# Optimization experiments

Hardware: AMD Instinct MI355X
Metric: run time of the kernel (lower is better)

Reference implementation:

```python
import jax, jax.numpy as jnp
import numpy as np

B, N, M = 2, 2048, 2048
D = 1024          # query_dim == context_dim == inner_dim
H, DH = 16, 64    # heads, dim_head
SCALE = DH ** -0.5


def setup_inputs() -> dict:
    key = jax.random.key(0)
    ks = jax.random.split(key, 7)
    s = 0.02
    return {
        "x": jax.random.normal(ks[0], (B, N, D), jnp.float32),
        "context": jax.random.normal(ks[1], (B, M, D), jnp.float32),
        "Wq": jax.random.normal(ks[2], (D, H * DH), jnp.float32) * s,
        "Wk": jax.random.normal(ks[3], (D, H * DH), jnp.float32) * s,
        "Wv": jax.random.normal(ks[4], (D, H * DH), jnp.float32) * s,
        "Wo": jax.random.normal(ks[5], (H * DH, D), jnp.float32) * s,
        "bo": jax.random.normal(ks[6], (D,), jnp.float32) * s,
    }


def reference(x, context, Wq, Wk, Wv, Wo, bo):
    # Linear projections (bias-free, as in to_q/to_k/to_v)
    q = (x @ Wq).reshape(B, N, H, DH)        # [B,N,H,DH]
    k = (context @ Wk).reshape(B, M, H, DH)  # [B,M,H,DH]
    v = (context @ Wv).reshape(B, M, H, DH)
    # QK^T * scale, softmax over keys, then AV
    sim = jnp.einsum('bnhd,bmhd->bhnm', q, k) * SCALE  # [B,H,N,M]
    attn = jax.nn.softmax(sim, axis=-1)
    out = jnp.einsum('bhnm,bmhd->bnhd', attn, v)       # [B,N,H,DH]
    out = out.reshape(B, N, H * DH)
    return out @ Wo + bo  # to_out Linear; dropout=0 is identity
```

## Files before the change

### kernel.cpp

```cpp
#include <hip/hip_runtime.h>

#define B_  2
#define N_  2048
#define M_  2048
#define D_  1024
#define H_  16
#define DH_ 64

typedef __bf16 bf16x8 __attribute__((ext_vector_type(8)));
typedef __bf16 bf16x4 __attribute__((ext_vector_type(4)));
typedef short  short4v __attribute__((ext_vector_type(4)));
typedef float  f32x4  __attribute__((ext_vector_type(4)));
typedef unsigned int u32x4v __attribute__((ext_vector_type(4)));

#define GAS(p) ((__attribute__((address_space(1))) void*)(p))
#define LAS(p) ((__attribute__((address_space(3))) void*)(p))

#define QPRESCALE 0.18033688011112042f

__device__ __forceinline__ unsigned short f2bf(float f) {
    unsigned int u = __builtin_bit_cast(unsigned int, f);
    u += 0x7fffu + ((u >> 16) & 1u);
    return (unsigned short)(u >> 16);
}

__device__ __forceinline__ unsigned cvtpkbf(float a, float b) {
    unsigned r;
    asm("v_cvt_pk_bf16_f32 %0, %1, %2" : "=v"(r) : "v"(a), "v"(b));
    return r;
}

__global__ __launch_bounds__(256) void prep(
    const float* __restrict__ x, const float* __restrict__ ctx,
    const float* __restrict__ Wq, const float* __restrict__ Wk,
    const float* __restrict__ Wv, const float* __restrict__ Wo,
    unsigned short* __restrict__ xb, unsigned short* __restrict__ cb,
    unsigned short* __restrict__ WTbase)
{
    if (blockIdx.z == 4) {
        int blk = blockIdx.y * 32 + blockIdx.x;
        int stride = 1024 * 256;
        for (int i = blk * 256 + threadIdx.x; i < 2097152; i += stride) {
            const float4* src; unsigned short* dst; int j;
            if (i < 1048576) { src = (const float4*)x;   dst = xb; j = i; }
            else             { src = (const float4*)ctx; dst = cb; j = i - 1048576; }
            float4 v = src[j];
            ushort4 o = make_ushort4(f2bf(v.x), f2bf(v.y), f2bf(v.z), f2bf(v.w));
            *(ushort4*)(dst + 4*j) = o;
        }
        return;
    }
    const float* W = (blockIdx.z == 0) ? Wq : (blockIdx.z == 1) ? Wk
                    : (blockIdx.z == 2) ? Wv : Wo;
    unsigned short* WT = WTbase + (size_t)blockIdx.z * 1048576;
    __shared__ unsigned short t[32][33];
    int tx = threadIdx.x & 31, ty8 = threadIdx.x >> 5;
    int c = blockIdx.x * 32 + tx;
#pragma unroll
    for (int i = 0; i < 4; ++i) {
        int r = blockIdx.y * 32 + i*8 + ty8;
        t[i*8 + ty8][tx] = f2bf(W[(size_t)r * 1024 + c]);
    }
    __syncthreads();
    int c2 = blockIdx.y * 32 + tx;
#pragma unroll
    for (int i = 0; i < 4; ++i) {
        int r2 = blockIdx.x * 32 + i*8 + ty8;
        WT[(size_t)r2 * 1024 + c2] = t[tx][i*8 + ty8];
    }
}

__global__ __launch_bounds__(256) void gemm128(
    const unsigned short* __restrict__ xb,
    const unsigned short* __restrict__ cb,
    const unsigned short* __restrict__ wT,
    const unsigned short* __restrict__ aoA,
    unsigned short* __restrict__ qkv_out,
    const float* __restrict__ bo,
    float* __restrict__ outF,
    int base_mode)
{
    __shared__ __align__(16) unsigned short As[128*32];
    __shared__ __align__(16) unsigned short Bs[128*32];

    const int mode = base_mode + blockIdx.z;
    const unsigned short* Amat;
    const unsigned short* Bt;
    if (mode == 0)      { Amat = wT;               Bt = xb; }
    else if (mode == 1) { Amat = wT + 1048576;     Bt = cb; }
    else if (mode == 2) { Amat = cb;               Bt = wT + 2*1048576; }
    else                { Amat = wT + 3*1048576;   Bt = aoA; }

    const int tid = threadIdx.x;
    const int w = tid >> 6, l = tid & 63;
    const int quad = l >> 4, l16 = l & 15;
    const int wm = w & 1, wn = w >> 1;
    int row0, col0;
    if (mode == 2) { row0 = blockIdx.x * 128; col0 = blockIdx.y * 128; }
    else           { row0 = blockIdx.y * 128; col0 = blockIdx.x * 128; }

    f32x4 acc[4][4];
#pragma unroll
    for (int i = 0; i < 4; ++i)
#pragma unroll
        for (int j = 0; j < 4; ++j) acc[i][j] = (f32x4){0.f, 0.f, 0.f, 0.f};

    for (int k0 = 0; k0 < 1024; k0 += 32) {
        __syncthreads();
#pragma unroll
        for (int i = 0; i < 2; ++i) {
            int s = i*256 + w*64 + l;
            int m = s >> 2, c = s & 3;
            int cs = c ^ ((m >> 1) & 3);
            __builtin_amdgcn_global_load_lds(
                GAS(Amat + (size_t)(row0 + m)*1024 + k0 + cs*8),
                LAS(As + (i*256 + w*64)*8), 16, 0, 0);
            __builtin_amdgcn_global_load_lds(
                GAS(Bt + (size_t)(col0 + m)*1024 + k0 + cs*8),
                LAS(Bs + (i*256 + w*64)*8), 16, 0, 0);
        }
        __syncthreads();

        bf16x8 af[4], bfr[4];
#pragma unroll
        for (int mt = 0; mt < 4; ++mt) {
            int m = wm*64 + mt*16 + l16;
            af[mt] = *reinterpret_cast<const bf16x8*>(As + m*32 + (quad ^ ((m >> 1) & 3))*8);
            int n = wn*64 + mt*16 + l16;
            bfr[mt] = *reinterpret_cast<const bf16x8*>(Bs + n*32 + (quad ^ ((n >> 1) & 3))*8);
        }
#pragma unroll
        for (int mt = 0; mt < 4; ++mt)
#pragma unroll
            for (int nt = 0; nt < 4; ++nt)
                acc[mt][nt] = __builtin_amdgcn_mfma_f32_16x16x32_bf16(
                    af[mt], bfr[nt], acc[mt][nt], 0, 0, 0);
    }

    if (mode == 3) {
#pragma unroll
        for (int mt = 0; mt < 4; ++mt) {
            int c = row0 + wm*64 + mt*16 + quad*4;
            float4 bv = *(const float4*)(bo + c);
#pragma unroll
            for (int nt = 0; nt < 4; ++nt) {
                int n = col0 + wn*64 + nt*16 + l16;
                float4 ov = make_float4(acc[mt][nt][0] + bv.x, acc[mt][nt][1] + bv.y,
                                        acc[mt][nt][2] + bv.z, acc[mt][nt][3] + bv.w);
                *(float4*)(outF + (size_t)n*1024 + c) = ov;
            }
        }
    } else if (mode == 2) {
#pragma unroll
        for (int mt = 0; mt < 4; ++mt) {
            int gr = row0 + wm*64 + mt*16 + quad*4;
            int b = gr >> 11, nidx = gr & 2047;
#pragma unroll
            for (int nt = 0; nt < 4; ++nt) {
                int col = col0 + wn*64 + nt*16 + l16;
                int h = col >> 6, d = col & 63;
                ushort4 pk = make_ushort4(f2bf(acc[mt][nt][0]), f2bf(acc[mt][nt][1]),
                                          f2bf(acc[mt][nt][2]), f2bf(acc[mt][nt][3]));
                *(ushort4*)(qkv_out + (size_t)2*4194304
                            + (size_t)((b*16 + h)*64 + d)*2048 + nidx) = pk;
            }
        }
    } else {
        const float qs = (mode == 0) ? QPRESCALE : 1.0f;
        unsigned short* obase = qkv_out + (size_t)mode*4194304;
#pragma unroll
        for (int nt = 0; nt < 4; ++nt) {
            int n = col0 + wn*64 + nt*16 + l16;
            int b = n >> 11, nidx = n & 2047;
#pragma unroll
            for (int mt = 0; mt < 4; ++mt) {
                int c = row0 + wm*64 + mt*16 + quad*4;
                int h = c >> 6, d = c & 63;
                ushort4 pkv = make_ushort4(
                    f2bf(acc[mt][nt][0] * qs), f2bf(acc[mt][nt][1] * qs),
                    f2bf(acc[mt][nt][2] * qs), f2bf(acc[mt][nt][3] * qs));
                *(ushort4*)(obase + (size_t)((b*16 + h)*2048 + nidx)*64 + d) = pkv;
            }
        }
    }
}

__global__ __launch_bounds__(256) void gemm_out(
    const unsigned short* __restrict__ woT,
    const unsigned short* __restrict__ aoA,
    const float* __restrict__ bo,
    float* __restrict__ outF)
{
    __shared__ __align__(16) unsigned short As[64*32];
    __shared__ __align__(16) unsigned short Bs[128*32];

    const int tid = threadIdx.x;
    const int w = tid >> 6, l = tid & 63;
    const int quad = l >> 4, l16 = l & 15;
    const int row0 = blockIdx.y * 64;
    const int col0 = blockIdx.x * 128;

    f32x4 acc[4][2];
#pragma unroll
    for (int i = 0; i < 4; ++i)
#pragma unroll
        for (int j = 0; j < 2; ++j) acc[i][j] = (f32x4){0.f, 0.f, 0.f, 0.f};

    for (int k0 = 0; k0 < 1024; k0 += 32) {
        __syncthreads();
        {
            int m = tid >> 2, c = tid & 3;
            int cs = c ^ ((m >> 1) & 3);
            __builtin_amdgcn_global_load_lds(
                GAS(woT + (size_t)(row0 + m)*1024 + k0 + cs*8),
                LAS(As + (w*64)*8), 16, 0, 0);
        }
#pragma unroll
        for (int i = 0; i < 2; ++i) {
            int s = i*256 + tid;
            int m = s >> 2, c = s & 3;
            int cs = c ^ ((m >> 1) & 3);
            __builtin_amdgcn_global_load_lds(
                GAS(aoA + (size_t)(col0 + m)*1024 + k0 + cs*8),
                LAS(Bs + (i*256 + w*64)*8), 16, 0, 0);
        }
        __syncthreads();

        bf16x8 af[4], bfr[2];
#pragma unroll
        for (int mt = 0; mt < 4; ++mt) {
            int m = mt*16 + l16;
            af[mt] = *reinterpret_cast<const bf16x8*>(As + m*32 + (quad ^ ((m >> 1) & 3))*8);
        }
#pragma unroll
        for (int nt = 0; nt < 2; ++nt) {
            int n = w*32 + nt*16 + l16;
            bfr[nt] = *reinterpret_cast<const bf16x8*>(Bs + n*32 + (quad ^ ((n >> 1) & 3))*8);
        }
#pragma unroll
        for (int mt = 0; mt < 4; ++mt)
#pragma unroll
            for (int nt = 0; nt < 2; ++nt)
                acc[mt][nt] = __builtin_amdgcn_mfma_f32_16x16x32_bf16(
                    af[mt], bfr[nt], acc[mt][nt], 0, 0, 0);
    }

#pragma unroll
    for (int mt = 0; mt < 4; ++mt) {
        int c = row0 + mt*16 + quad*4;
        float4 bv = *(const float4*)(bo + c);
#pragma unroll
        for (int nt = 0; nt < 2; ++nt) {
            int n = col0 + w*32 + nt*16 + l16;
            float4 ov = make_float4(acc[mt][nt][0] + bv.x, acc[mt][nt][1] + bv.y,
                                    acc[mt][nt][2] + bv.z, acc[mt][nt][3] + bv.w);
            *(float4*)(outF + (size_t)n*1024 + c) = ov;
        }
    }
}

__global__ __launch_bounds__(256, 2) void flash_attn(
    const unsigned short* __restrict__ qw,
    const unsigned short* __restrict__ kw,
    const unsigned short* __restrict__ vtw,
    unsigned short* __restrict__ ao)
{
    __shared__ __align__(16) unsigned short Tile[2][9216];

    const int tid = threadIdx.x;
    const int w = tid >> 6, l = tid & 63;
    const int quad = l >> 4, l16 = l & 15;
    const int bh = blockIdx.z * H_ + blockIdx.y;
    const int q0 = blockIdx.x * 128 + w * 32;

    int goff[5];
#pragma unroll
    for (int i = 0; i < 5; ++i) {
        int n = i*256 + w*64 + l;
        int m = (n < 576) ? n : n - 576;
        int row = m / 9, c = m % 9;  if (c > 7) c = 7;
        goff[i] = (n < 576) ? row*64 + c*8 : row*2048 + c*8;
    }
    const unsigned short* kbase = kw + (size_t)bh*131072;
    const unsigned short* vbase = vtw + (size_t)bh*131072;

    bf16x8 qf[2][2];
#pragma unroll
    for (int qg = 0; qg < 2; ++qg)
#pragma unroll
        for (int s = 0; s < 2; ++s)
            qf[qg][s] = *reinterpret_cast<const bf16x8*>(
                qw + (size_t)(bh*2048 + q0 + qg*16 + l16)*64 + s*32 + quad*8);

    f32x4 accO[2][4];
#pragma unroll
    for (int qg = 0; qg < 2; ++qg)
#pragma unroll
        for (int td = 0; td < 4; ++td) accO[qg][td] = (f32x4){0.f, 0.f, 0.f, 0.f};
    float lpart[2] = {0.f, 0.f};

    const f32x4 zz = (f32x4){0.f, 0.f, 0.f, 0.f};

    {
#pragma unroll
        for (int i = 0; i < 4; ++i) {
            const unsigned short* bp = (i*4 + w < 9) ? kbase : vbase;
            __builtin_amdgcn_global_load_lds(GAS(bp + goff[i]),
                LAS(&Tile[0][(i*256 + w*64)*8]), 16, 0, 0);
        }
        if (w < 2)
            __builtin_amdgcn_global_load_lds(GAS(vbase + goff[4]),
                LAS(&Tile[0][(1024 + w*64)*8]), 16, 0, 0);
    }

    for (int it = 0; it < 32; ++it) {
        __syncthreads();
        const int cur = it & 1;

        if (it + 1 < 32) {
            const unsigned short* kp = kbase + (it+1)*4096;
            const unsigned short* vp = vbase + (it+1)*64;
#pragma unroll
            for (int i = 0; i < 4; ++i) {
                const unsigned short* bp = (i*4 + w < 9) ? kp : vp;
                __builtin_amdgcn_global_load_lds(GAS(bp + goff[i]),
                    LAS(&Tile[cur^1][(i*256 + w*64)*8]), 16, 0, 0);
            }
            if (w < 2)
                __builtin_amdgcn_global_load_lds(GAS(vp + goff[4]),
                    LAS(&Tile[cur^1][(1024 + w*64)*8]), 16, 0, 0);
        }

        const unsigned short* Ks = &Tile[cur][0];
        const unsigned short* Vs = &Tile[cur][4608];

        f32x4 sac[2][4];
        __builtin_amdgcn_s_setprio(1);
#pragma unroll
        for (int t = 0; t < 4; ++t) {
            const unsigned short* krow = Ks + (t*16 + l16)*72 + quad*8;
            bf16x8 kf0 = *reinterpret_cast<const bf16x8*>(krow);
            bf16x8 kf1 = *reinterpret_cast<const bf16x8*>(krow + 32);
            sac[0][t] = __builtin_amdgcn_mfma_f32_16x16x32_bf16(kf0, qf[0][0], zz, 0, 0, 0);
            sac[1][t] = __builtin_amdgcn_mfma_f32_16x16x32_bf16(kf0, qf[1][0], zz, 0, 0, 0);
            sac[0][t] = __builtin_amdgcn_mfma_f32_16x16x32_bf16(kf1, qf[0][1], sac[0][t], 0, 0, 0);
            sac[1][t] = __builtin_amdgcn_mfma_f32_16x16x32_bf16(kf1, qf[1][1], sac[1][t], 0, 0, 0);
        }
        __builtin_amdgcn_s_setprio(0);

        u32x4v pB[2][2];
#pragma unroll
        for (int qg = 0; qg < 2; ++qg) {
            float s0 = 0.f, s1 = 0.f, s2 = 0.f, s3 = 0.f;
#pragma unroll
            for (int t2 = 0; t2 < 2; ++t2) {
                float pe0 = __builtin_amdgcn_exp2f(sac[qg][2*t2][0]);
                float pe1 = __builtin_amdgcn_exp2f(sac[qg][2*t2][1]);
                float pe2 = __builtin_amdgcn_exp2f(sac[qg][2*t2][2]);
                float pe3 = __builtin_amdgcn_exp2f(sac[qg][2*t2][3]);
                float po0 = __builtin_amdgcn_exp2f(sac[qg][2*t2+1][0]);
                float po1 = __builtin_amdgcn_exp2f(sac[qg][2*t2+1][1]);
                float po2 = __builtin_amdgcn_exp2f(sac[qg][2*t2+1][2]);
                float po3 = __builtin_amdgcn_exp2f(sac[qg][2*t2+1][3]);
                s0 += pe0 + po0; s1 += pe1 + po1;
                s2 += pe2 + po2; s3 += pe3 + po3;
                unsigned b0 = cvtpkbf(pe0, pe1), b1 = cvtpkbf(pe2, pe3);
                unsigned b2 = cvtpkbf(po0, po1), b3 = cvtpkbf(po2, po3);
                asm("v_permlane32_swap_b32 %0, %1" : "+v"(b0), "+v"(b2));
                asm("v_permlane16_swap_b32 %0, %1" : "+v"(b0), "+v"(b2));
                asm("v_permlane32_swap_b32 %0, %1" : "+v"(b1), "+v"(b3));
                asm("v_permlane16_swap_b32 %0, %1" : "+v"(b1), "+v"(b3));
                pB[qg][t2] = (u32x4v){b0, b1, b2, b3};
            }
            lpart[qg] += (s0 + s1) + (s2 + s3);
        }

        __builtin_amdgcn_s_setprio(1);
#pragma unroll
        for (int td = 0; td < 4; ++td) {
            const unsigned short* vrow = Vs + (td*16 + l16)*72 + quad*8;
#pragma unroll
            for (int t2 = 0; t2 < 2; ++t2) {
                bf16x8 vf = *reinterpret_cast<const bf16x8*>(vrow + t2*32);
                accO[0][td] = __builtin_amdgcn_mfma_f32_16x16x32_bf16(
                    vf, __builtin_bit_cast(bf16x8, pB[0][t2]), accO[0][td], 0, 0, 0);
                accO[1][td] = __builtin_amdgcn_mfma_f32_16x16x32_bf16(
                    vf, __builtin_bit_cast(bf16x8, pB[1][t2]), accO[1][td], 0, 0, 0);
            }
        }
        __builtin_amdgcn_s_setprio(0);
    }

#pragma unroll
    for (int qg = 0; qg < 2; ++qg) {
        float s = lpart[qg];
        s += __shfl_xor(s, 16);
        s += __shfl_xor(s, 32);
        float inv = 1.f / s;
        const size_t rowbase =
            (size_t)(blockIdx.z*2048 + q0 + qg*16 + l16)*1024 + blockIdx.y*64;
#pragma unroll
        for (int td = 0; td < 4; ++td)
#pragma unroll
            for (int r = 0; r < 4; ++r)
                ao[rowbase + td*16 + quad*4 + r] = f2bf(accO[qg][td][r] * inv);
    }
}

extern "C" void kernel_launch(void* const* d_in, const int* in_sizes, int n_in,
                              void* d_out, int out_size, void* d_ws, size_t ws_size,
                              hipStream_t stream)
{
    const float* x   = (const float*)d_in[0];
    const float* ctx = (const float*)d_in[1];
    const float* Wq  = (const float*)d_in[2];
    const float* Wk  = (const float*)d_in[3];
    const float* Wv  = (const float*)d_in[4];
    const float* Wo  = (const float*)d_in[5];
    const float* bo  = (const float*)d_in[6];
    float* out = (float*)d_out;

    unsigned short* ws  = (unsigned short*)d_ws;
    unsigned short* xb  = ws;
    unsigned short* cb  = ws + 4194304;
    unsigned short* wT  = ws + 8388608;
    unsigned short* qkv = ws + 12582912;
    unsigned short* ao  = ws;

    prep<<<dim3(32, 32, 5), dim3(256), 0, stream>>>(x, ctx, Wq, Wk, Wv, Wo, xb, cb, wT);
    gemm128<<<dim3(32, 8, 3), dim3(256), 0, stream>>>(xb, cb, wT, ao, qkv, bo, out, 0);
    flash_attn<<<dim3(16, 16, 2), dim3(256), 0, stream>>>(qkv, qkv + 4194304, qkv + 8388608, ao);
    gemm_out<<<dim3(32, 16), dim3(256), 0, stream>>>(wT + 3*1048576, ao, bo, out);
}
```

Measured before the change: 204.0 us.

## Load K/V fragments directly from global into registers, drop LDS staging

The flash attention kernel no longer stages K and V tiles through double-buffered shared memory with global_load_lds and block barriers. Each wave now loads its K fragments straight into registers, software-pipelined one tile ahead via ping-pong register arrays, and loads V fragments directly from global memory each iteration. This removes the __syncthreads and LDS traffic, but every wave now fetches the same K/V data independently and raises register pressure. It also deletes the mode==3 output-projection epilogue from the generic GEMM, which looks like dead-code cleanup.

```diff
diff --git a/kernel.cpp b/kernel.cpp
--- a/kernel.cpp
+++ b/kernel.cpp
@@ -137,20 +137,7 @@
                     af[mt], bfr[nt], acc[mt][nt], 0, 0, 0);
     }
 
-    if (mode == 3) {
-#pragma unroll
-        for (int mt = 0; mt < 4; ++mt) {
-            int c = row0 + wm*64 + mt*16 + quad*4;
-            float4 bv = *(const float4*)(bo + c);
-#pragma unroll
-            for (int nt = 0; nt < 4; ++nt) {
-                int n = col0 + wn*64 + nt*16 + l16;
-                float4 ov = make_float4(acc[mt][nt][0] + bv.x, acc[mt][nt][1] + bv.y,
-                                        acc[mt][nt][2] + bv.z, acc[mt][nt][3] + bv.w);
-                *(float4*)(outF + (size_t)n*1024 + c) = ov;
-            }
-        }
-    } else if (mode == 2) {
+    if (mode == 2) {
 #pragma unroll
         for (int mt = 0; mt < 4; ++mt) {
             int gr = row0 + wm*64 + mt*16 + quad*4;
@@ -265,24 +252,16 @@
     const unsigned short* __restrict__ vtw,
     unsigned short* __restrict__ ao)
 {
-    __shared__ __align__(16) unsigned short Tile[2][9216];
-
     const int tid = threadIdx.x;
     const int w = tid >> 6, l = tid & 63;
     const int quad = l >> 4, l16 = l & 15;
     const int bh = blockIdx.z * H_ + blockIdx.y;
     const int q0 = blockIdx.x * 128 + w * 32;
 
-    int goff[5];
-#pragma unroll
-    for (int i = 0; i < 5; ++i) {
-        int n = i*256 + w*64 + l;
-        int m = (n < 576) ? n : n - 576;
-        int row = m / 9, c = m % 9;  if (c > 7) c = 7;
-        goff[i] = (n < 576) ? row*64 + c*8 : row*2048 + c*8;
-    }
     const unsigned short* kbase = kw + (size_t)bh*131072;
     const unsigned short* vbase = vtw + (size_t)bh*131072;
+    const unsigned short* kf_base = kbase + (size_t)l16*64 + quad*8;
+    const unsigned short* vf_base = vbase + (size_t)l16*2048 + quad*8;
 
     bf16x8 qf[2][2];
 #pragma unroll
@@ -301,52 +280,38 @@
 
     const f32x4 zz = (f32x4){0.f, 0.f, 0.f, 0.f};
 
-    {
-#pragma unroll
-        for (int i = 0; i < 4; ++i) {
-            const unsigned short* bp = (i*4 + w < 9) ? kbase : vbase;
-            __builtin_amdgcn_global_load_lds(GAS(bp + goff[i]),
-                LAS(&Tile[0][(i*256 + w*64)*8]), 16, 0, 0);
-        }
-        if (w < 2)
-            __builtin_amdgcn_global_load_lds(GAS(vbase + goff[4]),
-                LAS(&Tile[0][(1024 + w*64)*8]), 16, 0, 0);
-    }
-
-    for (int it = 0; it < 32; ++it) {
-        __syncthreads();
-        const int cur = it & 1;
-
-        if (it + 1 < 32) {
-            const unsigned short* kp = kbase + (it+1)*4096;
-            const unsigned short* vp = vbase + (it+1)*64;
-#pragma unroll
-            for (int i = 0; i < 4; ++i) {
-                const unsigned short* bp = (i*4 + w < 9) ? kp : vp;
-                __builtin_amdgcn_global_load_lds(GAS(bp + goff[i]),
-                    LAS(&Tile[cur^1][(i*256 + w*64)*8]), 16, 0, 0);
-            }
-            if (w < 2)
-                __builtin_amdgcn_global_load_lds(GAS(vp + goff[4]),
-                    LAS(&Tile[cur^1][(1024 + w*64)*8]), 16, 0, 0);
-        }
-
-        const unsigned short* Ks = &Tile[cur][0];
-        const unsigned short* Vs = &Tile[cur][4608];
+    bf16x8 kA[4][2], kB[4][2];
+
+    auto load_k = [&](int it, bf16x8 (&kd)[4][2]) {
+#pragma unroll
+        for (int t = 0; t < 4; ++t)
+#pragma unroll
+            for (int kh = 0; kh < 2; ++kh)
+                kd[t][kh] = *reinterpret_cast<const bf16x8*>(
+                    kf_base + (size_t)(it*64 + t*16)*64 + kh*32);
+    };
+
+    auto tile = [&](int it, bf16x8 (&kC)[4][2], bf16x8 (&kN)[4][2]) {
+        bf16x8 vb[4][2];
+#pragma unroll
+        for (int td = 0; td < 4; ++td)
+#pragma unroll
+            for (int t2 = 0; t2 < 2; ++t2)
+                vb[td][t2] = *reinterpret_cast<const bf16x8*>(
+                    vf_base + (size_t)td*32768 + it*64 + t2*32);
 
         f32x4 sac[2][4];
         __builtin_amdgcn_s_setprio(1);
 #pragma unroll
         for (int t = 0; t < 4; ++t) {
-            const unsigned short* krow = Ks + (t*16 + l16)*72 + quad*8;
-            bf16x8 kf0 = *reinterpret_cast<const bf16x8*>(krow);
-            bf16x8 kf1 = *reinterpret_cast<const bf16x8*>(krow + 32);
-            sac[0][t] = __builtin_amdgcn_mfma_f32_16x16x32_bf16(kf0, qf[0][0], zz, 0, 0, 0);
-            sac[1][t] = __builtin_amdgcn_mfma_f32_16x16x32_bf16(kf0, qf[1][0], zz, 0, 0, 0);
-            sac[0][t] = __builtin_amdgcn_mfma_f32_16x16x32_bf16(kf1, qf[0][1], sac[0][t], 0, 0, 0);
-            sac[1][t] = __builtin_amdgcn_mfma_f32_16x16x32_bf16(kf1, qf[1][1], sac[1][t], 0, 0, 0);
+            sac[0][t] = __builtin_amdgcn_mfma_f32_16x16x32_bf16(kC[t][0], qf[0][0], zz, 0, 0, 0);
+            sac[1][t] = __builtin_amdgcn_mfma_f32_16x16x32_bf16(kC[t][0], qf[1][0], zz, 0, 0, 0);
+            sac[0][t] = __builtin_amdgcn_mfma_f32_16x16x32_bf16(kC[t][1], qf[0][1], sac[0][t], 0, 0, 0);
+            sac[1][t] = __builtin_amdgcn_mfma_f32_16x16x32_bf16(kC[t][1], qf[1][1], sac[1][t], 0, 0, 0);
         }
         __builtin_amdgcn_s_setprio(0);
+
+        if (it + 1 < 32) load_k(it + 1, kN);
 
         u32x4v pB[2][2];
 #pragma unroll
@@ -378,17 +343,21 @@
         __builtin_amdgcn_s_setprio(1);
 #pragma unroll
         for (int td = 0; td < 4; ++td) {
-            const unsigned short* vrow = Vs + (td*16 + l16)*72 + quad*8;
 #pragma unroll
             for (int t2 = 0; t2 < 2; ++t2) {
-                bf16x8 vf = *reinterpret_cast<const bf16x8*>(vrow + t2*32);
                 accO[0][td] = __builtin_amdgcn_mfma_f32_16x16x32_bf16(
-                    vf, __builtin_bit_cast(bf16x8, pB[0][t2]), accO[0][td], 0, 0, 0);
+                    vb[td][t2], __builtin_bit_cast(bf16x8, pB[0][t2]), accO[0][td], 0, 0, 0);
                 accO[1][td] = __builtin_amdgcn_mfma_f32_16x16x32_bf16(
-                    vf, __builtin_bit_cast(bf16x8, pB[1][t2]), accO[1][td], 0, 0, 0);
+                    vb[td][t2], __builtin_bit_cast(bf16x8, pB[1][t2]), accO[1][td], 0, 0, 0);
             }
         }
         __builtin_amdgcn_s_setprio(0);
+    };
+
+    load_k(0, kA);
+    for (int it2 = 0; it2 < 16; ++it2) {
+        tile(2*it2,     kA, kB);
+        tile(2*it2 + 1, kB, kA);
     }
 
 #pragma unroll
```

Measured after the change: 268.6 us. 31.7% more time.
